# Kernel tuning notes

Measured on AMD Instinct MI355X. Metric: run time of the kernel, lower is better.

Reference implementation:

```python
import jax, jax.numpy as jnp
import numpy as np

BN_EPS = 1e-5


def setup_inputs() -> dict:
    key = jax.random.key(0)
    ks = jax.random.split(key, 12)
    B, T, S = 8, 256, 64
    D = 256  # 2*u, u=128
    sc = lambda fan: 1.0 / np.sqrt(fan)
    return {
        "Hx": jax.random.normal(ks[0], (B, T, D), dtype=jnp.float32),
        "Hs": jax.random.normal(ks[1], (S, D), dtype=jnp.float32),
        # transformS = BatchNorm1d(D) -> Linear(D,D) -> ReLU -> Linear(D,D)
        "bn_gamma": jnp.ones((D,), jnp.float32),
        "bn_beta": jnp.zeros((D,), jnp.float32),
        "s_w1": jax.random.normal(ks[2], (D, D), jnp.float32) * sc(D),
        "s_b1": jnp.zeros((D,), jnp.float32),
        "s_w2": jax.random.normal(ks[3], (D, D), jnp.float32) * sc(D),
        "s_b2": jnp.zeros((D,), jnp.float32),
        # W = Linear(3D, D) -> ReLU -> Linear(D, 1)   (6u = 3D features)
        "w_w1": jax.random.normal(ks[4], (3 * D, D), jnp.float32) * sc(3 * D),
        "w_b1": jnp.zeros((D,), jnp.float32),
        "w_w2": jax.random.normal(ks[5], (D, 1), jnp.float32) * sc(D),
        "w_b2": jnp.zeros((1,), jnp.float32),
        "truthSeqY": jax.random.randint(ks[6], (B, T, S), 0, 2, dtype=jnp.int32),
        "inputLen": jax.random.randint(ks[7], (B,), 1, T, dtype=jnp.int32),
    }


def reference(Hx, Hs, bn_gamma, bn_beta, s_w1, s_b1, s_w2, s_b2,
              w_w1, w_b1, w_w2, w_b2, truthSeqY, inputLen):
    B, T, D = Hx.shape
    S = Hs.shape[0]

    # transformS: BatchNorm1d (training-mode batch stats over slot dim) + 2-layer MLP
    mu = jnp.mean(Hs, axis=0)
    var = jnp.var(Hs, axis=0)  # biased, as torch BN uses for normalization
    hs = (Hs - mu) * jax.lax.rsqrt(var + BN_EPS) * bn_gamma + bn_beta
    transHs = jax.nn.relu(hs @ s_w1 + s_b1) @ s_w2 + s_b2  # [S, D]

    # pairwise broadcast: cat(Hx, transHs, Hx*transHs) over [B,T,S,3D]
    mx = jnp.broadcast_to(Hx[:, :, None, :], (B, T, S, D))
    ms = jnp.broadcast_to(transHs[None, None, :, :], (B, T, S, D))
    feat = jnp.concatenate([mx, ms, mx * ms], axis=-1)  # [B,T,S,3D]

    # scoring MLP -> scalar per (token, slot)
    h = jax.nn.relu(feat @ w_w1 + w_b1)        # [B,T,S,D]
    atten = (h @ w_w2 + w_b2)[..., 0]          # [B,T,S]

    atten_score = jax.nn.softmax(atten, axis=2)             # softmax over slots
    G = jnp.einsum('bts,sd->btd', atten_score, transHs)     # weighted slot agg
    outputU = jnp.concatenate([Hx, G + Hx], axis=2)         # [B,T,2D]
    return outputU, atten_score
```

## Files before the change

kernel.cpp:

```cpp
#include <hip/hip_runtime.h>
#include <math.h>

#define DD 256
#define SS 64
#define BT 2048

typedef __attribute__((ext_vector_type(4))) float f32x4;
typedef __attribute__((ext_vector_type(8))) short bf16x8;
typedef __attribute__((ext_vector_type(4))) unsigned int u32x4;

typedef __attribute__((address_space(3))) unsigned lds_u32;
typedef const __attribute__((address_space(1))) unsigned glb_u32;

__device__ inline unsigned pack_bf16(float a, float b) {
    unsigned ua = __builtin_bit_cast(unsigned, a);
    unsigned ub = __builtin_bit_cast(unsigned, b);
    ua = (ua + 0x7fffu + ((ua >> 16) & 1u)) >> 16;
    ub = (ub + 0x7fffu + ((ub >> 16) & 1u)) >> 16;
    return ua | (ub << 16);
}

__global__ __launch_bounds__(1024) void
k_prep_apack(const float* __restrict__ Hs, const float* __restrict__ g,
             const float* __restrict__ b, const float* __restrict__ s_w1,
             const float* __restrict__ s_b1, const float* __restrict__ s_w2,
             const float* __restrict__ s_b2, const float* __restrict__ w_w1,
             const float* __restrict__ w_b1, const float* __restrict__ Hx,
             float* __restrict__ transHs, float* __restrict__ S1b,
             unsigned* __restrict__ Apack) {
    if (blockIdx.x >= 64) {
        int idx = (blockIdx.x - 64) * 1024 + threadIdx.x;
        int lane = idx & 63, ks = (idx >> 6) & 7, MT = idx >> 9;
        int t  = MT * 16 + (lane & 15);
        int k0 = ks * 32 + (lane >> 4) * 8;
        const float* src = Hx + t * DD + k0;
        float4 x0 = *(const float4*)src;
        float4 x1 = *(const float4*)(src + 4);
        unsigned p[4];
        p[0] = pack_bf16(x0.x, x0.y);
        p[1] = pack_bf16(x0.z, x0.w);
        p[2] = pack_bf16(x1.x, x1.y);
        p[3] = pack_bf16(x1.z, x1.w);
        *(u32x4*)(Apack + idx * 4) = *(const u32x4*)p;
        return;
    }
    __shared__ float rowA[DD], rowB[DD], rowC[DD];
    __shared__ float red[8][DD];
    const int s = blockIdx.x;
    const int j = threadIdx.x & 255, kw = threadIdx.x >> 8;
    float sum = 0.f, sumsq = 0.f;
#pragma unroll
    for (int s2 = kw * 16; s2 < kw * 16 + 16; ++s2) {
        float v = Hs[s2 * DD + j];
        sum += v; sumsq += v * v;
    }
    red[kw][j] = sum; red[4 + kw][j] = sumsq;
    __syncthreads();
    if (kw == 0) {
        float st = red[0][j] + red[1][j] + red[2][j] + red[3][j];
        float sq = red[4][j] + red[5][j] + red[6][j] + red[7][j];
        float mu  = st * (1.f / SS);
        float var = sq * (1.f / SS) - mu * mu;
        rowA[j] = (Hs[s * DD + j] - mu) * rsqrtf(var + 1e-5f) * g[j] + b[j];
    }
    __syncthreads();
    float a1 = 0.f;
#pragma unroll 16
    for (int d = kw * 64; d < kw * 64 + 64; ++d)
        a1 = fmaf(rowA[d], s_w1[d * DD + j], a1);
    red[kw][j] = a1;
    __syncthreads();
    if (kw == 0)
        rowB[j] = fmaxf(red[0][j] + red[1][j] + red[2][j] + red[3][j] + s_b1[j], 0.f);
    __syncthreads();
    float a2 = 0.f;
#pragma unroll 16
    for (int d = kw * 64; d < kw * 64 + 64; ++d)
        a2 = fmaf(rowB[d], s_w2[d * DD + j], a2);
    red[kw][j] = a2;
    __syncthreads();
    if (kw == 0) {
        float r = red[0][j] + red[1][j] + red[2][j] + red[3][j] + s_b2[j];
        rowC[j] = r;
        transHs[s * DD + j] = r;
    }
    __syncthreads();
    float a3 = 0.f;
#pragma unroll 16
    for (int d = kw * 64; d < kw * 64 + 64; ++d)
        a3 = fmaf(rowC[d], w_w1[(256 + d) * DD + j], a3);
    red[kw][j] = a3;
    __syncthreads();
    if (kw == 0)
        S1b[s * DD + j] = red[0][j] + red[1][j] + red[2][j] + red[3][j] + w_b1[j];
}

__global__ __launch_bounds__(256) void
k_pack_bs(const float* __restrict__ w_w1, const float* __restrict__ transHs,
          unsigned* __restrict__ Bs) {
    __shared__ float ms_l[16][DD];
    const int ic = blockIdx.x & 31, sg = blockIdx.x >> 5;
    const int s0 = sg * 16;
    const int tid = threadIdx.x;
#pragma unroll
    for (int i = 0; i < 4; ++i) {
        int e4 = i * 256 + tid;
        ((float4*)ms_l)[e4] = ((const float4*)(transHs + s0 * DD))[e4];
    }
    __syncthreads();
    const int idx = ic * 256 + tid;
    const int lane = idx & 63, ks = (idx >> 6) & 7, nt = idx >> 9;
    const int j  = nt * 16 + (lane & 15);
    const int k0 = ks * 32 + (lane >> 4) * 8;
    const float* C = w_w1 + 512 * DD;
    float w1v[8], cv[8];
#pragma unroll
    for (int e = 0; e < 8; ++e) {
        w1v[e] = w_w1[(k0 + e) * DD + j];
        cv[e]  = C[(k0 + e) * DD + j];
    }
    for (int ss = 0; ss < 16; ++ss) {
        unsigned p[4];
#pragma unroll
        for (int e = 0; e < 4; ++e) {
            float f0 = w1v[2 * e]     + ms_l[ss][k0 + 2 * e]     * cv[2 * e];
            float f1 = w1v[2 * e + 1] + ms_l[ss][k0 + 2 * e + 1] * cv[2 * e + 1];
            p[e] = pack_bf16(f0, f1);
        }
        *(u32x4*)(Bs + ((s0 + ss) * 8192 + idx) * 4) = *(const u32x4*)p;
    }
}

__global__ __launch_bounds__(256, 2) void
k_main_mfma(const unsigned* __restrict__ Apack, const unsigned* __restrict__ Bs,
            const float* __restrict__ S1b, const float* __restrict__ w2,
            const float* __restrict__ w_b2, float* __restrict__ atten) {
    __shared__ unsigned Albs[16384];
    const int swz  = (blockIdx.x & 7) * 128 + (blockIdx.x >> 3);
    const int s    = swz >> 4;
    const int tile = swz & 15;
    const int t0 = tile * 128;
    const int tid = threadIdx.x;
    const int w = tid >> 6, l = tid & 63;
    const int lrow = l & 15, lg = l >> 4;
    const unsigned* Asrc = Apack + tile * 16384;
    const unsigned* Bsl  = Bs + s * 32768;

#pragma unroll
    for (int i = 0; i < 16; ++i) {
        int chunk = w * 16 + i;
        __builtin_amdgcn_global_load_lds((glb_u32*)(Asrc + chunk * 256 + l * 4),
                                         (lds_u32*)(Albs + chunk * 256), 16, 0, 0);
    }
    __syncthreads();

    f32x4 acc[8][4] = {};
    bf16x8 af[2][8];
    bf16x8 bf[2][4];

#pragma unroll
    for (int mt = 0; mt < 8; ++mt)
        af[0][mt] = *(const bf16x8*)((const char*)Albs + ((mt * 8 + 0) * 64 + l) * 16);
#pragma unroll
    for (int nt = 0; nt < 4; ++nt)
        bf[0][nt] = *(const bf16x8*)(Bsl + (((w * 4 + nt) * 8 + 0) * 64 + l) * 4);

#pragma unroll
    for (int ks = 0; ks < 8; ++ks) {
        const int cur = ks & 1, nxt = cur ^ 1;
        if (ks < 7) {
#pragma unroll
            for (int mt = 0; mt < 8; ++mt)
                af[nxt][mt] = *(const bf16x8*)((const char*)Albs + ((mt * 8 + ks + 1) * 64 + l) * 16);
#pragma unroll
            for (int nt = 0; nt < 4; ++nt)
                bf[nxt][nt] = *(const bf16x8*)(Bsl + (((w * 4 + nt) * 8 + ks + 1) * 64 + l) * 4);
        }
#pragma unroll
        for (int nt = 0; nt < 4; ++nt)
#pragma unroll
            for (int mt = 0; mt < 8; ++mt)
                acc[mt][nt] = __builtin_amdgcn_mfma_f32_16x16x32_bf16(af[cur][mt], bf[cur][nt], acc[mt][nt], 0, 0, 0);
    }
    __syncthreads();

    float* attp = (float*)Albs;
    float s1[4], w2v[4];
#pragma unroll
    for (int nt = 0; nt < 4; ++nt) {
        int jn = (w * 4 + nt) * 16 + lrow;
        s1[nt]  = S1b[s * DD + jn];
        w2v[nt] = w2[jn];
    }
#pragma unroll
    for (int mt = 0; mt < 8; ++mt) {
#pragma unroll
        for (int i = 0; i < 4; ++i) {
            float p = 0.f;
#pragma unroll
            for (int nt = 0; nt < 4; ++nt) {
                float h = fmaxf(acc[mt][nt][i] + s1[nt], 0.f);
                p = fmaf(h, w2v[nt], p);
            }
            p += __shfl_xor(p, 1);
            p += __shfl_xor(p, 2);
            p += __shfl_xor(p, 4);
            p += __shfl_xor(p, 8);
            if (lrow == 0) attp[w * 128 + mt * 16 + lg * 4 + i] = p;
        }
    }
    __syncthreads();
    if (tid < 128) {
        float r = attp[tid] + attp[128 + tid] + attp[256 + tid] + attp[384 + tid] + w_b2[0];
        atten[(t0 + tid) * SS + s] = r;
    }
}

__global__ __launch_bounds__(256) void
k_out(const float* __restrict__ Hx, const float* __restrict__ m,
      const float* __restrict__ atten, float* __restrict__ outU,
      float* __restrict__ outA) {
    int wave = threadIdx.x >> 6, lane = threadIdx.x & 63;
    int t = blockIdx.x * 4 + wave;
    float a = atten[t * SS + lane];
    float mx = a;
#pragma unroll
    for (int off = 32; off; off >>= 1) mx = fmaxf(mx, __shfl_xor(mx, off));
    float e = __expf(a - mx);
    float sum = e;
#pragma unroll
    for (int off = 32; off; off >>= 1) sum += __shfl_xor(sum, off);
    float p = e / sum;
    outA[t * SS + lane] = p;
    float gacc[4] = {};
    for (int s = 0; s < SS; ++s) {
        float ps = __shfl(p, s);
#pragma unroll
        for (int q = 0; q < 4; ++q)
            gacc[q] = fmaf(ps, m[s * DD + lane + 64 * q], gacc[q]);
    }
#pragma unroll
    for (int q = 0; q < 4; ++q) {
        int j = lane + 64 * q;
        float x = Hx[t * DD + j];
        outU[t * 2 * DD + j] = x;
        outU[t * 2 * DD + DD + j] = x + gacc[q];
    }
}

extern "C" void kernel_launch(void* const* d_in, const int* in_sizes, int n_in,
                              void* d_out, int out_size, void* d_ws, size_t ws_size,
                              hipStream_t stream) {
    const float* Hx   = (const float*)d_in[0];
    const float* Hs   = (const float*)d_in[1];
    const float* bn_g = (const float*)d_in[2];
    const float* bn_b = (const float*)d_in[3];
    const float* s_w1 = (const float*)d_in[4];
    const float* s_b1 = (const float*)d_in[5];
    const float* s_w2 = (const float*)d_in[6];
    const float* s_b2 = (const float*)d_in[7];
    const float* w_w1 = (const float*)d_in[8];
    const float* w_b1 = (const float*)d_in[9];
    const float* w_w2 = (const float*)d_in[10];
    const float* w_b2 = (const float*)d_in[11];

    float* ws      = (float*)d_ws;
    float* transHs = ws;
    float* S1b     = ws + 16384;
    float* atten   = ws + 32768;
    unsigned* Apack = (unsigned*)(ws + 163840);
    unsigned* Bs    = Apack + 262144;

    float* outU = (float*)d_out;
    float* outA = outU + BT * 2 * DD;

    k_prep_apack<<<128, 1024, 0, stream>>>(Hs, bn_g, bn_b, s_w1, s_b1, s_w2, s_b2,
                                           w_w1, w_b1, Hx, transHs, S1b, Apack);
    k_pack_bs<<<128, 256, 0, stream>>>(w_w1, transHs, Bs);
    k_main_mfma<<<1024, 256, 0, stream>>>(Apack, Bs, S1b, w_w2, w_b2, atten);
    k_out<<<BT / 4, 256, 0, stream>>>(Hx, transHs, atten, outU, outA);
}
```

Before: 57.28 us.

## Process two slots per block to reuse the LDS-staged A tile

```diff
diff --git a/kernel.cpp b/kernel.cpp
--- a/kernel.cpp
+++ b/kernel.cpp
@@ -136,15 +136,18 @@
             const float* __restrict__ S1b, const float* __restrict__ w2,
             const float* __restrict__ w_b2, float* __restrict__ atten) {
     __shared__ unsigned Albs[16384];
-    const int swz  = (blockIdx.x & 7) * 128 + (blockIdx.x >> 3);
-    const int s    = swz >> 4;
-    const int tile = swz & 15;
+    __shared__ float attp[2][4][128];
+    const int bid = blockIdx.x;
+    const int xcd = bid & 7, li = bid >> 3;
+    const int sp  = xcd * 4 + (li >> 4);
+    const int tile = li & 15;
     const int t0 = tile * 128;
     const int tid = threadIdx.x;
     const int w = tid >> 6, l = tid & 63;
     const int lrow = l & 15, lg = l >> 4;
     const unsigned* Asrc = Apack + tile * 16384;
-    const unsigned* Bsl  = Bs + s * 32768;
+    const unsigned* Bp0 = Bs + (sp * 2 + 0) * 32768;
+    const unsigned* Bp1 = Bs + (sp * 2 + 1) * 32768;
 
 #pragma unroll
     for (int i = 0; i < 16; ++i) {
@@ -152,46 +155,79 @@
         __builtin_amdgcn_global_load_lds((glb_u32*)(Asrc + chunk * 256 + l * 4),
                                          (lds_u32*)(Albs + chunk * 256), 16, 0, 0);
     }
+
+    bf16x8 bf[2][4];
+#pragma unroll
+    for (int nt = 0; nt < 4; ++nt)
+        bf[0][nt] = *(const bf16x8*)(Bp0 + (((w * 4 + nt) * 8 + 0) * 64 + l) * 4);
+    float s1v[2][4], w2v[4];
+#pragma unroll
+    for (int nt = 0; nt < 4; ++nt) {
+        int jn = (w * 4 + nt) * 16 + lrow;
+        w2v[nt]    = w2[jn];
+        s1v[0][nt] = S1b[(sp * 2 + 0) * DD + jn];
+        s1v[1][nt] = S1b[(sp * 2 + 1) * DD + jn];
+    }
+    const float b2 = w_b2[0];
     __syncthreads();
 
     f32x4 acc[8][4] = {};
     bf16x8 af[2][8];
-    bf16x8 bf[2][4];
-
 #pragma unroll
     for (int mt = 0; mt < 8; ++mt)
         af[0][mt] = *(const bf16x8*)((const char*)Albs + ((mt * 8 + 0) * 64 + l) * 16);
-#pragma unroll
-    for (int nt = 0; nt < 4; ++nt)
-        bf[0][nt] = *(const bf16x8*)(Bsl + (((w * 4 + nt) * 8 + 0) * 64 + l) * 4);
-
-#pragma unroll
-    for (int ks = 0; ks < 8; ++ks) {
-        const int cur = ks & 1, nxt = cur ^ 1;
-        if (ks < 7) {
+
+#pragma unroll
+    for (int kk = 0; kk < 16; ++kk) {
+        const int cur = kk & 1, nxt = cur ^ 1;
+        if (kk < 15) {
+            const int nks = (kk + 1) & 7;
+            const unsigned* Bn = ((kk + 1) < 8) ? Bp0 : Bp1;
 #pragma unroll
             for (int mt = 0; mt < 8; ++mt)
-                af[nxt][mt] = *(const bf16x8*)((const char*)Albs + ((mt * 8 + ks + 1) * 64 + l) * 16);
+                af[nxt][mt] = *(const bf16x8*)((const char*)Albs + ((mt * 8 + nks) * 64 + l) * 16);
 #pragma unroll
             for (int nt = 0; nt < 4; ++nt)
-                bf[nxt][nt] = *(const bf16x8*)(Bsl + (((w * 4 + nt) * 8 + ks + 1) * 64 + l) * 4);
+                bf[nxt][nt] = *(const bf16x8*)(Bn + (((w * 4 + nt) * 8 + nks) * 64 + l) * 4);
         }
 #pragma unroll
         for (int nt = 0; nt < 4; ++nt)
 #pragma unroll
             for (int mt = 0; mt < 8; ++mt)
                 acc[mt][nt] = __builtin_amdgcn_mfma_f32_16x16x32_bf16(af[cur][mt], bf[cur][nt], acc[mt][nt], 0, 0, 0);
-    }
-    __syncthreads();
-
-    float* attp = (float*)Albs;
-    float s1[4], w2v[4];
-#pragma unroll
-    for (int nt = 0; nt < 4; ++nt) {
-        int jn = (w * 4 + nt) * 16 + lrow;
-        s1[nt]  = S1b[s * DD + jn];
-        w2v[nt] = w2[jn];
-    }
+
+        if (kk == 7) {
+#pragma unroll
+            for (int mt = 0; mt < 8; ++mt) {
+#pragma unroll
+                for (int i = 0; i < 4; ++i) {
+                    float p = 0.f;
+#pragma unroll
+                    for (int nt = 0; nt < 4; ++nt) {
+                        float h = fmaxf(acc[mt][nt][i] + s1v[0][nt], 0.f);
+                        p = fmaf(h, w2v[nt], p);
+                    }
+                    p += __shfl_xor(p, 1);
+                    p += __shfl_xor(p, 2);
+                    p += __shfl_xor(p, 4);
+                    p += __shfl_xor(p, 8);
+                    if (lrow == 0) attp[0][w][mt * 16 + lg * 4 + i] = p;
+                }
+            }
+            __syncthreads();
+            if (tid < 128) {
+                float r = attp[0][0][tid] + attp[0][1][tid] + attp[0][2][tid]
+                        + attp[0][3][tid] + b2;
+                atten[(t0 + tid) * SS + (sp * 2 + 0)] = r;
+            }
+#pragma unroll
+            for (int mt = 0; mt < 8; ++mt)
+#pragma unroll
+                for (int nt = 0; nt < 4; ++nt)
+                    acc[mt][nt] = (f32x4){0.f, 0.f, 0.f, 0.f};
+        }
+    }
+
 #pragma unroll
     for (int mt = 0; mt < 8; ++mt) {
 #pragma unroll
@@ -199,20 +235,21 @@
             float p = 0.f;
 #pragma unroll
             for (int nt = 0; nt < 4; ++nt) {
-                float h = fmaxf(acc[mt][nt][i] + s1[nt], 0.f);
+                float h = fmaxf(acc[mt][nt][i] + s1v[1][nt], 0.f);
                 p = fmaf(h, w2v[nt], p);
             }
             p += __shfl_xor(p, 1);
             p += __shfl_xor(p, 2);
             p += __shfl_xor(p, 4);
             p += __shfl_xor(p, 8);
-            if (lrow == 0) attp[w * 128 + mt * 16 + lg * 4 + i] = p;
+            if (lrow == 0) attp[1][w][mt * 16 + lg * 4 + i] = p;
         }
     }
     __syncthreads();
     if (tid < 128) {
-        float r = attp[tid] + attp[128 + tid] + attp[256 + tid] + attp[384 + tid] + w_b2[0];
-        atten[(t0 + tid) * SS + s] = r;
+        float r = attp[1][0][tid] + attp[1][1][tid] + attp[1][2][tid]
+                + attp[1][3][tid] + b2;
+        atten[(t0 + tid) * SS + (sp * 2 + 1)] = r;
     }
 }
 
@@ -277,6 +314,6 @@
     k_prep_apack<<<128, 1024, 0, stream>>>(Hs, bn_g, bn_b, s_w1, s_b1, s_w2, s_b2,
                                            w_w1, w_b1, Hx, transHs, S1b, Apack);
     k_pack_bs<<<128, 256, 0, stream>>>(w_w1, transHs, Bs);
-    k_main_mfma<<<1024, 256, 0, stream>>>(Apack, Bs, S1b, w_w2, w_b2, atten);
+    k_main_mfma<<<512, 256, 0, stream>>>(Apack, Bs, S1b, w_w2, w_b2, atten);
     k_out<<<BT / 4, 256, 0, stream>>>(Hx, transHs, atten, outU, outA);
 }
```

Measured after the change: 60.75 us. +6.1%, slower.

## Split transform prep and merge S1b, Apack and Bs packing into one launch

Applied to the files above, without the earlier changes.

```diff
diff --git a/kernel.cpp b/kernel.cpp
--- a/kernel.cpp
+++ b/kernel.cpp
@@ -21,15 +21,73 @@
 }
 
 __global__ __launch_bounds__(1024) void
-k_prep_apack(const float* __restrict__ Hs, const float* __restrict__ g,
-             const float* __restrict__ b, const float* __restrict__ s_w1,
-             const float* __restrict__ s_b1, const float* __restrict__ s_w2,
-             const float* __restrict__ s_b2, const float* __restrict__ w_w1,
-             const float* __restrict__ w_b1, const float* __restrict__ Hx,
-             float* __restrict__ transHs, float* __restrict__ S1b,
-             unsigned* __restrict__ Apack) {
-    if (blockIdx.x >= 64) {
-        int idx = (blockIdx.x - 64) * 1024 + threadIdx.x;
+k_trans(const float* __restrict__ Hs, const float* __restrict__ g,
+        const float* __restrict__ b, const float* __restrict__ s_w1,
+        const float* __restrict__ s_b1, const float* __restrict__ s_w2,
+        const float* __restrict__ s_b2, float* __restrict__ transHs) {
+    __shared__ float rowA[DD], rowB[DD];
+    __shared__ float red[8][DD];
+    const int s = blockIdx.x;
+    const int j = threadIdx.x & 255, kw = threadIdx.x >> 8;
+    float sum = 0.f, sumsq = 0.f;
+#pragma unroll
+    for (int s2 = kw * 16; s2 < kw * 16 + 16; ++s2) {
+        float v = Hs[s2 * DD + j];
+        sum += v; sumsq += v * v;
+    }
+    red[kw][j] = sum; red[4 + kw][j] = sumsq;
+    __syncthreads();
+    if (kw == 0) {
+        float st = red[0][j] + red[1][j] + red[2][j] + red[3][j];
+        float sq = red[4][j] + red[5][j] + red[6][j] + red[7][j];
+        float mu  = st * (1.f / SS);
+        float var = sq * (1.f / SS) - mu * mu;
+        rowA[j] = (Hs[s * DD + j] - mu) * rsqrtf(var + 1e-5f) * g[j] + b[j];
+    }
+    __syncthreads();
+    float a1 = 0.f;
+#pragma unroll 16
+    for (int d = kw * 64; d < kw * 64 + 64; ++d)
+        a1 = fmaf(rowA[d], s_w1[d * DD + j], a1);
+    red[kw][j] = a1;
+    __syncthreads();
+    if (kw == 0)
+        rowB[j] = fmaxf(red[0][j] + red[1][j] + red[2][j] + red[3][j] + s_b1[j], 0.f);
+    __syncthreads();
+    float a2 = 0.f;
+#pragma unroll 16
+    for (int d = kw * 64; d < kw * 64 + 64; ++d)
+        a2 = fmaf(rowB[d], s_w2[d * DD + j], a2);
+    red[kw][j] = a2;
+    __syncthreads();
+    if (kw == 0)
+        transHs[s * DD + j] = red[0][j] + red[1][j] + red[2][j] + red[3][j] + s_b2[j];
+}
+
+__global__ __launch_bounds__(1024) void
+k_stage(const float* __restrict__ w_w1, const float* __restrict__ w_b1,
+        const float* __restrict__ Hx, const float* __restrict__ transHs,
+        float* __restrict__ S1b, unsigned* __restrict__ Apack,
+        unsigned* __restrict__ Bs) {
+    const int bid = blockIdx.x;
+    const int tid = threadIdx.x;
+    if (bid < 64) {
+        __shared__ float rowC[DD];
+        __shared__ float red[4][DD];
+        const int s = bid;
+        const int j = tid & 255, kw = tid >> 8;
+        if (kw == 0) rowC[j] = transHs[s * DD + j];
+        __syncthreads();
+        float a3 = 0.f;
+#pragma unroll 16
+        for (int d = kw * 64; d < kw * 64 + 64; ++d)
+            a3 = fmaf(rowC[d], w_w1[(256 + d) * DD + j], a3);
+        red[kw][j] = a3;
+        __syncthreads();
+        if (kw == 0)
+            S1b[s * DD + j] = red[0][j] + red[1][j] + red[2][j] + red[3][j] + w_b1[j];
+    } else if (bid < 128) {
+        int idx = (bid - 64) * 1024 + tid;
         int lane = idx & 63, ks = (idx >> 6) & 7, MT = idx >> 9;
         int t  = MT * 16 + (lane & 15);
         int k0 = ks * 32 + (lane >> 4) * 8;
@@ -42,92 +100,38 @@
         p[2] = pack_bf16(x1.x, x1.y);
         p[3] = pack_bf16(x1.z, x1.w);
         *(u32x4*)(Apack + idx * 4) = *(const u32x4*)p;
-        return;
-    }
-    __shared__ float rowA[DD], rowB[DD], rowC[DD];
-    __shared__ float red[8][DD];
-    const int s = blockIdx.x;
-    const int j = threadIdx.x & 255, kw = threadIdx.x >> 8;
-    float sum = 0.f, sumsq = 0.f;
-#pragma unroll
-    for (int s2 = kw * 16; s2 < kw * 16 + 16; ++s2) {
-        float v = Hs[s2 * DD + j];
-        sum += v; sumsq += v * v;
-    }
-    red[kw][j] = sum; red[4 + kw][j] = sumsq;
-    __syncthreads();
-    if (kw == 0) {
-        float st = red[0][j] + red[1][j] + red[2][j] + red[3][j];
-        float sq = red[4][j] + red[5][j] + red[6][j] + red[7][j];
-        float mu  = st * (1.f / SS);
-        float var = sq * (1.f / SS) - mu * mu;
-        rowA[j] = (Hs[s * DD + j] - mu) * rsqrtf(var + 1e-5f) * g[j] + b[j];
-    }
-    __syncthreads();
-    float a1 = 0.f;
-#pragma unroll 16
-    for (int d = kw * 64; d < kw * 64 + 64; ++d)
-        a1 = fmaf(rowA[d], s_w1[d * DD + j], a1);
-    red[kw][j] = a1;
-    __syncthreads();
-    if (kw == 0)
-        rowB[j] = fmaxf(red[0][j] + red[1][j] + red[2][j] + red[3][j] + s_b1[j], 0.f);
-    __syncthreads();
-    float a2 = 0.f;
-#pragma unroll 16
-    for (int d = kw * 64; d < kw * 64 + 64; ++d)
-        a2 = fmaf(rowB[d], s_w2[d * DD + j], a2);
-    red[kw][j] = a2;
-    __syncthreads();
-    if (kw == 0) {
-        float r = red[0][j] + red[1][j] + red[2][j] + red[3][j] + s_b2[j];
-        rowC[j] = r;
-        transHs[s * DD + j] = r;
-    }
-    __syncthreads();
-    float a3 = 0.f;
-#pragma unroll 16
-    for (int d = kw * 64; d < kw * 64 + 64; ++d)
-        a3 = fmaf(rowC[d], w_w1[(256 + d) * DD + j], a3);
-    red[kw][j] = a3;
-    __syncthreads();
-    if (kw == 0)
-        S1b[s * DD + j] = red[0][j] + red[1][j] + red[2][j] + red[3][j] + w_b1[j];
-}
-
-__global__ __launch_bounds__(256) void
-k_pack_bs(const float* __restrict__ w_w1, const float* __restrict__ transHs,
-          unsigned* __restrict__ Bs) {
-    __shared__ float ms_l[16][DD];
-    const int ic = blockIdx.x & 31, sg = blockIdx.x >> 5;
-    const int s0 = sg * 16;
-    const int tid = threadIdx.x;
-#pragma unroll
-    for (int i = 0; i < 4; ++i) {
-        int e4 = i * 256 + tid;
-        ((float4*)ms_l)[e4] = ((const float4*)(transHs + s0 * DD))[e4];
-    }
-    __syncthreads();
-    const int idx = ic * 256 + tid;
-    const int lane = idx & 63, ks = (idx >> 6) & 7, nt = idx >> 9;
-    const int j  = nt * 16 + (lane & 15);
-    const int k0 = ks * 32 + (lane >> 4) * 8;
-    const float* C = w_w1 + 512 * DD;
-    float w1v[8], cv[8];
-#pragma unroll
-    for (int e = 0; e < 8; ++e) {
-        w1v[e] = w_w1[(k0 + e) * DD + j];
-        cv[e]  = C[(k0 + e) * DD + j];
-    }
-    for (int ss = 0; ss < 16; ++ss) {
-        unsigned p[4];
-#pragma unroll
-        for (int e = 0; e < 4; ++e) {
-            float f0 = w1v[2 * e]     + ms_l[ss][k0 + 2 * e]     * cv[2 * e];
-            float f1 = w1v[2 * e + 1] + ms_l[ss][k0 + 2 * e + 1] * cv[2 * e + 1];
-            p[e] = pack_bf16(f0, f1);
-        }
-        *(u32x4*)(Bs + ((s0 + ss) * 8192 + idx) * 4) = *(const u32x4*)p;
+    } else {
+        __shared__ float ms_l[16][DD];
+        const int b2 = bid - 128;
+        const int ic = b2 & 7, sg = b2 >> 3;
+        const int s0 = sg * 16;
+#pragma unroll
+        for (int i = 0; i < 4; ++i) {
+            int e4 = i * 1024 + tid;
+            if (e4 < 1024) ((float4*)ms_l)[e4] = ((const float4*)(transHs + s0 * DD))[e4];
+        }
+        __syncthreads();
+        const int idx = ic * 1024 + tid;
+        const int lane = idx & 63, ks = (idx >> 6) & 7, nt = idx >> 9;
+        const int j  = nt * 16 + (lane & 15);
+        const int k0 = ks * 32 + (lane >> 4) * 8;
+        const float* C = w_w1 + 512 * DD;
+        float w1v[8], cv[8];
+#pragma unroll
+        for (int e = 0; e < 8; ++e) {
+            w1v[e] = w_w1[(k0 + e) * DD + j];
+            cv[e]  = C[(k0 + e) * DD + j];
+        }
+        for (int ss = 0; ss < 16; ++ss) {
+            unsigned p[4];
+#pragma unroll
+            for (int e = 0; e < 4; ++e) {
+                float f0 = w1v[2 * e]     + ms_l[ss][k0 + 2 * e]     * cv[2 * e];
+                float f1 = w1v[2 * e + 1] + ms_l[ss][k0 + 2 * e + 1] * cv[2 * e + 1];
+                p[e] = pack_bf16(f0, f1);
+            }
+            *(u32x4*)(Bs + ((s0 + ss) * 8192 + idx) * 4) = *(const u32x4*)p;
+        }
     }
 }
 
@@ -176,11 +180,13 @@
             for (int nt = 0; nt < 4; ++nt)
                 bf[nxt][nt] = *(const bf16x8*)(Bsl + (((w * 4 + nt) * 8 + ks + 1) * 64 + l) * 4);
         }
+        __builtin_amdgcn_s_setprio(1);
 #pragma unroll
         for (int nt = 0; nt < 4; ++nt)
 #pragma unroll
             for (int mt = 0; mt < 8; ++mt)
                 acc[mt][nt] = __builtin_amdgcn_mfma_f32_16x16x32_bf16(af[cur][mt], bf[cur][nt], acc[mt][nt], 0, 0, 0);
+        __builtin_amdgcn_s_setprio(0);
     }
     __syncthreads();
 
@@ -274,9 +280,8 @@
     float* outU = (float*)d_out;
     float* outA = outU + BT * 2 * DD;
 
-    k_prep_apack<<<128, 1024, 0, stream>>>(Hs, bn_g, bn_b, s_w1, s_b1, s_w2, s_b2,
-                                           w_w1, w_b1, Hx, transHs, S1b, Apack);
-    k_pack_bs<<<128, 256, 0, stream>>>(w_w1, transHs, Bs);
+    k_trans<<<SS, 1024, 0, stream>>>(Hs, bn_g, bn_b, s_w1, s_b1, s_w2, s_b2, transHs);
+    k_stage<<<160, 1024, 0, stream>>>(w_w1, w_b1, Hx, transHs, S1b, Apack, Bs);
     k_main_mfma<<<1024, 256, 0, stream>>>(Apack, Bs, S1b, w_w2, w_b2, atten);
     k_out<<<BT / 4, 256, 0, stream>>>(Hx, transHs, atten, outU, outA);
 }
```

After: 54.75 us, median of 2. -4.4%, faster.
